# Kernel optimization log

Hardware: AMD Instinct MI355X
Metric: run time of the kernel (lower is better)

Reference implementation:

```python
import jax, jax.numpy as jnp
import numpy as np

HEADS = 8
NUM_QUERY = 16

def setup_inputs() -> dict:
    key = jax.random.key(0)
    k1, k2, k3 = jax.random.split(key, 3)
    b, t, h, w, C = 8, 16, 32, 32, 256  # C = heads * c, c = 32
    q = NUM_QUERY
    btn_features = 256
    btn_enc = jax.random.normal(k1, (b, t, h, w, C), dtype=jnp.float32)
    btn_dec = jax.random.normal(k2, (b, q * t, C), dtype=jnp.float32)
    W = jax.random.normal(k3, (HEADS * q, btn_features), dtype=jnp.float32) * (1.0 / np.sqrt(HEADS * q))
    bias = jnp.zeros((btn_features,), dtype=jnp.float32)
    return {"btn_dec": btn_dec, "btn_enc": btn_enc, "W": W, "bias": bias}

def reference(btn_dec, btn_enc, W, bias):
    b, t, h, w, C = btn_enc.shape
    g = HEADS
    c = C // g
    q = btn_dec.shape[1] // t
    # b t h w (g c) -> b g t h w c
    enc = btn_enc.reshape(b, t, h, w, g, c).transpose(0, 4, 1, 2, 3, 5)
    # b (q t) (g c) -> b g q t c
    dec = btn_dec.reshape(b, q, t, g, c).transpose(0, 3, 1, 2, 4)
    # broadcast-mul + sum over c == batched contraction; output ordered (..., q, g)
    scores = jnp.einsum('bgqtc,bgthwc->bthwqg', dec, enc)  # [b,t,h,w,q,g]
    scores = scores.reshape(b, t * h * w, q * g)
    out = jax.nn.relu(scores @ W + bias)  # [b, t*h*w, btn_features]
    return out.reshape(b, t, h, w, -1)
```

## Files before the change

kernel.cpp:

```cpp
#include <hip/hip_runtime.h>


#define CCH 256
#define FF  256
#define HW  1024

typedef __bf16 bf16x8 __attribute__((ext_vector_type(8)));
typedef float  f32x4  __attribute__((ext_vector_type(4)));
typedef float  f32x16 __attribute__((ext_vector_type(16)));
typedef unsigned short u16x4 __attribute__((ext_vector_type(4)));
typedef unsigned short u16x8 __attribute__((ext_vector_type(8)));

__device__ __forceinline__ unsigned short f2bf(float f) {
    __bf16 b = (__bf16)f;
    return __builtin_bit_cast(unsigned short, b);
}

__device__ __forceinline__ void gload_lds16(const unsigned short* g, unsigned short* l) {
    __builtin_amdgcn_global_load_lds(
        (const __attribute__((address_space(1))) unsigned int*)g,
        (__attribute__((address_space(3))) unsigned int*)l, 16, 0, 0);
}

__global__ __launch_bounds__(256) void compute_Mt_kernel(
        const float* __restrict__ dec, const float* __restrict__ W,
        unsigned short* __restrict__ Mt) {
    const int j  = blockIdx.x;
    const int bt = blockIdx.y;
    const int b  = bt >> 4, t = bt & 15;
    const int f  = threadIdx.x;
    __shared__ float ldec[16][64];

    const float* decbt = dec + (size_t)b * 65536 + (size_t)t * 256 + j * 64;
    {
        const int q = threadIdx.x >> 4, seg = threadIdx.x & 15;
        const float4 v = *reinterpret_cast<const float4*>(decbt + q * 4096 + seg * 4);
        *reinterpret_cast<float4*>(&ldec[q][seg * 4]) = v;
    }
    __syncthreads();

    u16x8 rv[8];
    #pragma unroll
    for (int gi = 0; gi < 2; ++gi) {
        const int g = j * 2 + gi;
        float wv[16];
        #pragma unroll
        for (int q = 0; q < 16; ++q) wv[q] = W[(q * 8 + g) * FF + f];
        #pragma unroll
        for (int cc = 0; cc < 32; ++cc) {
            float s = 0.f;
            #pragma unroll
            for (int q = 0; q < 16; ++q) s += ldec[q][gi * 32 + cc] * wv[q];
            const int idx = gi * 32 + cc;
            rv[idx >> 3][idx & 7] = f2bf(s);
        }
    }
    unsigned short* dst = Mt + (size_t)bt * (FF * CCH) + (size_t)f * CCH + j * 64;
    #pragma unroll
    for (int s = 0; s < 8; ++s)
        *reinterpret_cast<u16x8*>(dst + s * 8) = rv[s];
}

__global__ __launch_bounds__(512, 6) void gemm_tile_kernel(
        const float* __restrict__ E, const unsigned short* __restrict__ Mt,
        const float* __restrict__ bias, float* __restrict__ O) {
    const int id0 = blockIdx.x;
    const int id  = ((id0 & 7) << 8) | (id0 >> 3);
    const int bt = id >> 4;
    const int fq = (id >> 2) & 3;
    const int rg = id & 3;
    const int tid = threadIdx.x;
    const int lane = tid & 63, wq = tid >> 6;
    const int lr5 = lane & 31, kgr = lane >> 5;

    const float*          Ebt = E  + (size_t)bt * (HW * CCH);
    const unsigned short* Mtb = Mt + (size_t)bt * (FF * CCH) + (size_t)(fq * 64) * CCH;
    float*                Obt = O  + (size_t)bt * (HW * FF);

    __shared__ __align__(16) unsigned short Bs[64 * 256];
    __shared__ __align__(16) unsigned short Et[8][32 * 32];

    #pragma unroll
    for (int p = 0; p < 4; ++p) {
        const int g = p * 512 + tid;
        const int r = g >> 5, s = g & 31;
        gload_lds16(Mtb + (size_t)r * CCH + ((s ^ (r & 7)) * 8), &Bs[g * 8]);
    }
    __syncthreads();

    const int rowbase = rg * 256 + wq * 32;

    const float bv0 = bias[fq * 64 + lr5];
    const float bv1 = bias[fq * 64 + 32 + lr5];

    const int g_r8 = lane >> 3;
    const int g_s3 = lane & 7;
    const int bswz = lr5 & 7;
    const int eswz = lr5 & 3;
    const unsigned short* Bs0 = &Bs[lr5 * 256];
    const unsigned short* Bs1 = &Bs[(32 + lr5) * 256];
    unsigned short* Etw = &Et[wq][0];
    const unsigned short* Etr = &Etw[lr5 * 32];

    f32x4 Sva[4], Svb[4];
    f32x16 acc0, acc1;

    auto GLOAD = [&](int it, f32x4 (&S)[4]) {
        const float* base = Ebt + (size_t)rowbase * CCH + (it & 7) * 32 + g_s3 * 4;
        #pragma unroll
        for (int i = 0; i < 4; ++i)
            S[i] = *reinterpret_cast<const f32x4*>(base + (size_t)(i * 8 + g_r8) * CCH);
    };
    auto EWRITE = [&](const f32x4 (&S)[4]) {
        #pragma unroll
        for (int i = 0; i < 4; ++i) {
            const int r = i * 8 + g_r8;
            u16x4 h = { f2bf(S[i][0]), f2bf(S[i][1]), f2bf(S[i][2]), f2bf(S[i][3]) };
            *reinterpret_cast<u16x4*>(
                &Etw[r * 32 + (((g_s3 >> 1) ^ (r & 3)) * 8) + (g_s3 & 1) * 4]) = h;
        }
    };
    auto COMPUTE = [&](int it) {
        const int kc = it & 7;
        if (kc == 0) { acc0 = (f32x16)0.f; acc1 = (f32x16)0.f; }
        #pragma unroll
        for (int kk = 0; kk < 2; ++kk) {
            const bf16x8 af = *reinterpret_cast<const bf16x8*>(
                &Etr[((kk * 2 + kgr) ^ eswz) * 8]);
            const bf16x8 b0 = *reinterpret_cast<const bf16x8*>(
                &Bs0[((kc * 4 + kk * 2 + kgr) ^ bswz) * 8]);
            const bf16x8 b1 = *reinterpret_cast<const bf16x8*>(
                &Bs1[((kc * 4 + kk * 2 + kgr) ^ bswz) * 8]);
            acc0 = __builtin_amdgcn_mfma_f32_32x32x16_bf16(af, b0, acc0, 0, 0, 0);
            acc1 = __builtin_amdgcn_mfma_f32_32x32x16_bf16(af, b1, acc1, 0, 0, 0);
        }
        if (kc == 7) {
            const int row0 = rowbase + 4 * kgr;
            #pragma unroll
            for (int reg = 0; reg < 16; ++reg) {
                const int r = row0 + (reg & 3) + 8 * (reg >> 2);
                float* op = Obt + (size_t)r * FF + fq * 64 + lr5;
                __builtin_nontemporal_store(fmaxf(acc0[reg] + bv0, 0.f), op);
                __builtin_nontemporal_store(fmaxf(acc1[reg] + bv1, 0.f), op + 32);
            }
        }
    };

    GLOAD(0, Sva);
    GLOAD(1, Svb);
    EWRITE(Sva);
    for (int itp = 0; itp < 8; itp += 2) {
        COMPUTE(itp);
        if (itp + 2 < 8) GLOAD(itp + 2, Sva);
        EWRITE(Svb);
        COMPUTE(itp + 1);
        if (itp + 3 < 8) GLOAD(itp + 3, Svb);
        if (itp + 2 < 8) EWRITE(Sva);
    }
}

extern "C" void kernel_launch(void* const* d_in, const int* in_sizes, int n_in,
                              void* d_out, int out_size, void* d_ws, size_t ws_size,
                              hipStream_t stream) {
    const float* dec  = (const float*)d_in[0];
    const float* enc  = (const float*)d_in[1];
    const float* W    = (const float*)d_in[2];
    const float* bias = (const float*)d_in[3];
    float* out = (float*)d_out;
    unsigned short* Mt = (unsigned short*)d_ws;

    compute_Mt_kernel<<<dim3(4, 128), dim3(256), 0, stream>>>(dec, W, Mt);
    gemm_tile_kernel<<<dim3(2048), dim3(512), 0, stream>>>(enc, Mt, bias, out);
}
```

Baseline: 59.69 us.

## Widen GEMM tile to 128 output features per block to halve E reloads

Each block now computes 128 output features instead of 64, using four MFMA accumulators per wave and a 64 KB B tile in LDS. The grid halves to 1024 blocks, so each fp32 encoder row block is read from global memory and converted to bf16 twice instead of four times. In exchange it uses more LDS and registers per block, lowers occupancy (launch bounds 6 to 4) and leaves fewer blocks to spread across CUs.

```diff
diff --git a/kernel.cpp b/kernel.cpp
--- a/kernel.cpp
+++ b/kernel.cpp
@@ -61,27 +61,27 @@
         *reinterpret_cast<u16x8*>(dst + s * 8) = rv[s];
 }
 
-__global__ __launch_bounds__(512, 6) void gemm_tile_kernel(
+__global__ __launch_bounds__(512, 4) void gemm_tile_kernel(
         const float* __restrict__ E, const unsigned short* __restrict__ Mt,
         const float* __restrict__ bias, float* __restrict__ O) {
     const int id0 = blockIdx.x;
-    const int id  = ((id0 & 7) << 8) | (id0 >> 3);
-    const int bt = id >> 4;
-    const int fq = (id >> 2) & 3;
+    const int id  = ((id0 & 7) << 7) | (id0 >> 3);
+    const int bt = id >> 3;
+    const int fh = (id >> 2) & 1;
     const int rg = id & 3;
     const int tid = threadIdx.x;
     const int lane = tid & 63, wq = tid >> 6;
     const int lr5 = lane & 31, kgr = lane >> 5;
 
     const float*          Ebt = E  + (size_t)bt * (HW * CCH);
-    const unsigned short* Mtb = Mt + (size_t)bt * (FF * CCH) + (size_t)(fq * 64) * CCH;
+    const unsigned short* Mtb = Mt + (size_t)bt * (FF * CCH) + (size_t)(fh * 128) * CCH;
     float*                Obt = O  + (size_t)bt * (HW * FF);
 
-    __shared__ __align__(16) unsigned short Bs[64 * 256];
+    __shared__ __align__(16) unsigned short Bs[128 * 256];
     __shared__ __align__(16) unsigned short Et[8][32 * 32];
 
     #pragma unroll
-    for (int p = 0; p < 4; ++p) {
+    for (int p = 0; p < 8; ++p) {
         const int g = p * 512 + tid;
         const int r = g >> 5, s = g & 31;
         gload_lds16(Mtb + (size_t)r * CCH + ((s ^ (r & 7)) * 8), &Bs[g * 8]);
@@ -90,20 +90,22 @@
 
     const int rowbase = rg * 256 + wq * 32;
 
-    const float bv0 = bias[fq * 64 + lr5];
-    const float bv1 = bias[fq * 64 + 32 + lr5];
+    float bv[4];
+    #pragma unroll
+    for (int fn = 0; fn < 4; ++fn) bv[fn] = bias[fh * 128 + fn * 32 + lr5];
 
     const int g_r8 = lane >> 3;
     const int g_s3 = lane & 7;
     const int bswz = lr5 & 7;
     const int eswz = lr5 & 3;
-    const unsigned short* Bs0 = &Bs[lr5 * 256];
-    const unsigned short* Bs1 = &Bs[(32 + lr5) * 256];
+    const unsigned short* Bsp[4];
+    #pragma unroll
+    for (int fn = 0; fn < 4; ++fn) Bsp[fn] = &Bs[(fn * 32 + lr5) * 256];
     unsigned short* Etw = &Et[wq][0];
     const unsigned short* Etr = &Etw[lr5 * 32];
 
     f32x4 Sva[4], Svb[4];
-    f32x16 acc0, acc1;
+    f32x16 acc0, acc1, acc2, acc3;
 
     auto GLOAD = [&](int it, f32x4 (&S)[4]) {
         const float* base = Ebt + (size_t)rowbase * CCH + (it & 7) * 32 + g_s3 * 4;
@@ -122,26 +124,34 @@
     };
     auto COMPUTE = [&](int it) {
         const int kc = it & 7;
-        if (kc == 0) { acc0 = (f32x16)0.f; acc1 = (f32x16)0.f; }
+        if (kc == 0) {
+            acc0 = (f32x16)0.f; acc1 = (f32x16)0.f;
+            acc2 = (f32x16)0.f; acc3 = (f32x16)0.f;
+        }
         #pragma unroll
         for (int kk = 0; kk < 2; ++kk) {
             const bf16x8 af = *reinterpret_cast<const bf16x8*>(
                 &Etr[((kk * 2 + kgr) ^ eswz) * 8]);
-            const bf16x8 b0 = *reinterpret_cast<const bf16x8*>(
-                &Bs0[((kc * 4 + kk * 2 + kgr) ^ bswz) * 8]);
-            const bf16x8 b1 = *reinterpret_cast<const bf16x8*>(
-                &Bs1[((kc * 4 + kk * 2 + kgr) ^ bswz) * 8]);
-            acc0 = __builtin_amdgcn_mfma_f32_32x32x16_bf16(af, b0, acc0, 0, 0, 0);
-            acc1 = __builtin_amdgcn_mfma_f32_32x32x16_bf16(af, b1, acc1, 0, 0, 0);
+            const int bo = ((kc * 4 + kk * 2 + kgr) ^ bswz) * 8;
+            acc0 = __builtin_amdgcn_mfma_f32_32x32x16_bf16(
+                af, *reinterpret_cast<const bf16x8*>(&Bsp[0][bo]), acc0, 0, 0, 0);
+            acc1 = __builtin_amdgcn_mfma_f32_32x32x16_bf16(
+                af, *reinterpret_cast<const bf16x8*>(&Bsp[1][bo]), acc1, 0, 0, 0);
+            acc2 = __builtin_amdgcn_mfma_f32_32x32x16_bf16(
+                af, *reinterpret_cast<const bf16x8*>(&Bsp[2][bo]), acc2, 0, 0, 0);
+            acc3 = __builtin_amdgcn_mfma_f32_32x32x16_bf16(
+                af, *reinterpret_cast<const bf16x8*>(&Bsp[3][bo]), acc3, 0, 0, 0);
         }
         if (kc == 7) {
             const int row0 = rowbase + 4 * kgr;
             #pragma unroll
             for (int reg = 0; reg < 16; ++reg) {
                 const int r = row0 + (reg & 3) + 8 * (reg >> 2);
-                float* op = Obt + (size_t)r * FF + fq * 64 + lr5;
-                __builtin_nontemporal_store(fmaxf(acc0[reg] + bv0, 0.f), op);
-                __builtin_nontemporal_store(fmaxf(acc1[reg] + bv1, 0.f), op + 32);
+                float* op = Obt + (size_t)r * FF + fh * 128 + lr5;
+                __builtin_nontemporal_store(fmaxf(acc0[reg] + bv[0], 0.f), op);
+                __builtin_nontemporal_store(fmaxf(acc1[reg] + bv[1], 0.f), op + 32);
+                __builtin_nontemporal_store(fmaxf(acc2[reg] + bv[2], 0.f), op + 64);
+                __builtin_nontemporal_store(fmaxf(acc3[reg] + bv[3], 0.f), op + 96);
             }
         }
     };
@@ -170,5 +180,5 @@
     unsigned short* Mt = (unsigned short*)d_ws;
 
     compute_Mt_kernel<<<dim3(4, 128), dim3(256), 0, stream>>>(dec, W, Mt);
-    gemm_tile_kernel<<<dim3(2048), dim3(512), 0, stream>>>(enc, Mt, bias, out);
+    gemm_tile_kernel<<<dim3(1024), dim3(512), 0, stream>>>(enc, Mt, bias, out);
 }
```

New measurement: 58.26 us (median of 2 runs). -2.4%, faster.
